# Performance work log

Measured on AMD Instinct MI355X. Metric: run time of the kernel, lower is better.

The kernel has to match this reference:

```python
import jax, jax.numpy as jnp
import numpy as np
from math import sqrt

N = 50000      # n_nodes
M = 800000     # n_edges (avg degree 16)
D = 256        # d_Embedding
H = 8          # heads
DK = 32        # per-head key/query dim
DV = 32        # per-head value dim


def setup_inputs() -> dict:
    key = jax.random.key(0)
    ks = jax.random.split(key, 10)
    s = 0.02
    x = jax.random.normal(ks[0], (N, D), dtype=jnp.float32)
    edge_index = jax.random.randint(ks[1], (2, M), 0, N, dtype=jnp.int32)
    # projection weights stored pre-reshaped to (D, H, dhead); equivalent to nn.Linear(D, H*dhead)
    Wk = jax.random.normal(ks[2], (D, H, DK), dtype=jnp.float32) * s
    bk = jax.random.normal(ks[3], (H, DK), dtype=jnp.float32) * s
    Wq = jax.random.normal(ks[4], (D, H, DK), dtype=jnp.float32) * s
    bq = jax.random.normal(ks[5], (H, DK), dtype=jnp.float32) * s
    Wv = jax.random.normal(ks[6], (D, H, DV), dtype=jnp.float32) * s
    bv = jax.random.normal(ks[7], (H, DV), dtype=jnp.float32) * s
    Wagg = jax.random.normal(ks[8], (H * DV, D), dtype=jnp.float32) * s
    bagg = jnp.zeros((D,), dtype=jnp.float32)
    Wff = jax.random.normal(ks[9], (D, D), dtype=jnp.float32) * s
    bff = jnp.zeros((D,), dtype=jnp.float32)
    return {"x": x, "edge_index": edge_index, "Wk": Wk, "bk": bk, "Wq": Wq,
            "bq": bq, "Wv": Wv, "bv": bv, "Wagg": Wagg, "bagg": bagg,
            "Wff": Wff, "bff": bff}


def reference(x, edge_index, Wk, bk, Wq, bq, Wv, bv, Wagg, bagg, Wff, bff):
    recv = edge_index[0]
    send = edge_index[1]
    # per-head projections: (N, H, d)
    K = jnp.einsum('nd,dhk->nhk', x, Wk) + bk
    Q = jnp.einsum('nd,dhk->nhk', x, Wq) + bq
    V = jnp.einsum('nd,dhv->nhv', x, Wv) + bv
    # edge-wise attention logits: (M, H)
    qk = jnp.sum(Q[recv] * K[send], axis=-1)
    # faithful to original: rescale by 3/global_max, then exp
    att = jnp.exp(qk * 3.0 / jnp.max(qk))
    # segment-softmax normalization over edges sharing a receiver
    sums = jax.ops.segment_sum(att, recv, num_segments=N)  # (N, H)
    att = att / sums[recv] / sqrt(DK)
    # weighted scatter-add of sender values: (N, H, DV)
    msg = att[..., None] * V[send]
    out = jax.ops.segment_sum(msg, recv, num_segments=N)
    out = jax.nn.relu(out).reshape(N, H * DV)
    out = jax.nn.relu(out @ Wagg + bagg)
    out = jax.nn.relu(out @ Wff + bff)
    return x + out
```

## Files before the change

kernel.cpp:

```cpp
#include <hip/hip_runtime.h>

#define N_NODES 50000
#define M_EDGES 800000
#define RP 50048

typedef __bf16 bf16x8 __attribute__((ext_vector_type(8)));
typedef __bf16 bf16x4 __attribute__((ext_vector_type(4)));
typedef float  f32x4  __attribute__((ext_vector_type(4)));

static __device__ __forceinline__ unsigned enc_ord(float f) {
    unsigned b = __float_as_uint(f);
    return (b & 0x80000000u) ? ~b : (b | 0x80000000u);
}
static __device__ __forceinline__ float dec_ord(unsigned u) {
    unsigned b = (u & 0x80000000u) ? (u ^ 0x80000000u) : ~u;
    return __uint_as_float(b);
}
static __device__ __forceinline__ float bflo(unsigned u) { return __uint_as_float(u << 16); }
static __device__ __forceinline__ float bfhi(unsigned u) { return __uint_as_float(u & 0xffff0000u); }

__global__ void init_kernel(int* counts, int* cursor, unsigned* gmax) {
    int t = blockIdx.x * blockDim.x + threadIdx.x;
    if (t < N_NODES) { counts[t] = 0; cursor[t] = 0; }
    if (t == 0) *gmax = 0u;
}

__global__ void wsplit_kernel(const float* __restrict__ W,
                              __bf16* __restrict__ th, __bf16* __restrict__ tl) {
    int t = blockIdx.x * 256 + threadIdx.x;
    int n = t >> 8, k = t & 255;
    float v = W[(size_t)k * 256 + n];
    __bf16 h = (__bf16)v;
    th[t] = h;
    tl[t] = (__bf16)(v - (float)h);
}

__global__ void xsplit_kernel(const float* __restrict__ X,
                              __bf16* __restrict__ xh, __bf16* __restrict__ xl) {
    size_t i = ((size_t)blockIdx.x * 256 + threadIdx.x) * 4;
    if (i >= (size_t)N_NODES * 256) return;
    float4 v = *(const float4*)(X + i);
    bf16x4 hh, ll;
    hh[0] = (__bf16)v.x; ll[0] = (__bf16)(v.x - (float)hh[0]);
    hh[1] = (__bf16)v.y; ll[1] = (__bf16)(v.y - (float)hh[1]);
    hh[2] = (__bf16)v.z; ll[2] = (__bf16)(v.z - (float)hh[2]);
    hh[3] = (__bf16)v.w; ll[3] = (__bf16)(v.w - (float)hh[3]);
    *(bf16x4*)(xh + i) = hh;
    *(bf16x4*)(xl + i) = ll;
}

__global__ __launch_bounds__(256) void gemm_mfma(
    const __bf16* __restrict__ Ah, const __bf16* __restrict__ Al,
    const __bf16* __restrict__ Bth, const __bf16* __restrict__ Btl,
    const float* __restrict__ bias, const float* __restrict__ residual,
    float* __restrict__ C, __bf16* __restrict__ CbH, __bf16* __restrict__ CbL,
    int nrows, int do_relu) {
    __shared__ __attribute__((aligned(16))) __bf16 sAh[128 * 40];
    __shared__ __attribute__((aligned(16))) __bf16 sAl[128 * 40];
    __shared__ __attribute__((aligned(16))) __bf16 sBh[128 * 40];
    __shared__ __attribute__((aligned(16))) __bf16 sBl[128 * 40];

    int row0 = blockIdx.x * 128;
    int n0   = blockIdx.y * 128;
    int tid  = threadIdx.x;
    int lane = tid & 63, wave = tid >> 6;
    int wm = (wave >> 1) * 64, wn = (wave & 1) * 64;

    f32x4 acc[4][4];
    #pragma unroll
    for (int i = 0; i < 4; i++)
        #pragma unroll
        for (int j = 0; j < 4; j++) acc[i][j] = (f32x4)(0.f);

    int r  = tid >> 1;
    int hf = tid & 1;
    bool valid = (row0 + r) < nrows;

    for (int kk = 0; kk < 256; kk += 32) {
        {
            size_t ga = (size_t)(row0 + r) * 256 + kk + hf * 16;
            uint4 z = make_uint4(0u, 0u, 0u, 0u);
            uint4 ah0 = valid ? *(const uint4*)(Ah + ga)     : z;
            uint4 ah1 = valid ? *(const uint4*)(Ah + ga + 8) : z;
            uint4 al0 = valid ? *(const uint4*)(Al + ga)     : z;
            uint4 al1 = valid ? *(const uint4*)(Al + ga + 8) : z;
            *(uint4*)&sAh[r * 40 + hf * 16]     = ah0;
            *(uint4*)&sAh[r * 40 + hf * 16 + 8] = ah1;
            *(uint4*)&sAl[r * 40 + hf * 16]     = al0;
            *(uint4*)&sAl[r * 40 + hf * 16 + 8] = al1;
        }
        {
            size_t gb = (size_t)(n0 + r) * 256 + kk + hf * 16;
            uint4 vh0 = *(const uint4*)(Bth + gb);
            uint4 vh1 = *(const uint4*)(Bth + gb + 8);
            uint4 vl0 = *(const uint4*)(Btl + gb);
            uint4 vl1 = *(const uint4*)(Btl + gb + 8);
            *(uint4*)&sBh[r * 40 + hf * 16]     = vh0;
            *(uint4*)&sBh[r * 40 + hf * 16 + 8] = vh1;
            *(uint4*)&sBl[r * 40 + hf * 16]     = vl0;
            *(uint4*)&sBl[r * 40 + hf * 16 + 8] = vl1;
        }
        __syncthreads();

        int m_base = wm + (lane & 15);
        int n_base = wn + (lane & 15);
        int koff = (lane >> 4) * 8;
        bf16x8 ah[4], al[4], bh[4], bl[4];
        #pragma unroll
        for (int mt = 0; mt < 4; mt++) {
            ah[mt] = *(const bf16x8*)&sAh[(m_base + mt * 16) * 40 + koff];
            al[mt] = *(const bf16x8*)&sAl[(m_base + mt * 16) * 40 + koff];
        }
        #pragma unroll
        for (int nt = 0; nt < 4; nt++) {
            bh[nt] = *(const bf16x8*)&sBh[(n_base + nt * 16) * 40 + koff];
            bl[nt] = *(const bf16x8*)&sBl[(n_base + nt * 16) * 40 + koff];
        }
        #pragma unroll
        for (int mt = 0; mt < 4; mt++)
            #pragma unroll
            for (int nt = 0; nt < 4; nt++) {
                acc[mt][nt] = __builtin_amdgcn_mfma_f32_16x16x32_bf16(ah[mt], bh[nt], acc[mt][nt], 0, 0, 0);
                acc[mt][nt] = __builtin_amdgcn_mfma_f32_16x16x32_bf16(al[mt], bh[nt], acc[mt][nt], 0, 0, 0);
                acc[mt][nt] = __builtin_amdgcn_mfma_f32_16x16x32_bf16(ah[mt], bl[nt], acc[mt][nt], 0, 0, 0);
            }
        __syncthreads();
    }

    #pragma unroll
    for (int mt = 0; mt < 4; mt++) {
        #pragma unroll
        for (int nt = 0; nt < 4; nt++) {
            int col = n0 + wn + nt * 16 + (lane & 15);
            #pragma unroll
            for (int rr = 0; rr < 4; rr++) {
                int row = row0 + wm + mt * 16 + (lane >> 4) * 4 + rr;
                if (row < nrows) {
                    float v = acc[mt][nt][rr] + bias[col];
                    if (do_relu) v = fmaxf(v, 0.f);
                    size_t idx = (size_t)row * 256 + col;
                    if (CbH) {
                        __bf16 hh = (__bf16)v;
                        CbH[idx] = hh;
                        if (CbL) CbL[idx] = (__bf16)(v - (float)hh);
                    } else {
                        if (residual) v += residual[idx];
                        C[idx] = v;
                    }
                }
            }
        }
    }
}

__global__ void hist_kernel(const int* __restrict__ recv, int* __restrict__ counts) {
    int t = blockIdx.x * 256 + threadIdx.x;
    if (t < M_EDGES) atomicAdd(&counts[recv[t]], 1);
}

__global__ void scan_kernel(const int* __restrict__ counts, int* __restrict__ offsets) {
    __shared__ int part[256];
    int t = threadIdx.x;
    const int per = (N_NODES + 255) / 256;
    int start = t * per;
    int end = min(start + per, N_NODES);
    int s = 0;
    for (int i = start; i < end; i++) s += counts[i];
    part[t] = s;
    __syncthreads();
    if (t == 0) {
        int acc = 0;
        for (int i = 0; i < 256; i++) { int v = part[i]; part[i] = acc; acc += v; }
    }
    __syncthreads();
    int acc = part[t];
    for (int i = start; i < end; i++) { offsets[i] = acc; acc += counts[i]; }
    if (end == N_NODES && start < N_NODES) offsets[N_NODES] = acc;
}

__global__ void fill_kernel(const int* __restrict__ recv, const int* __restrict__ send,
                            const int* __restrict__ offsets,
                            int* __restrict__ cursor, int* __restrict__ ssorted,
                            int* __restrict__ rsorted) {
    int t = blockIdx.x * 256 + threadIdx.x;
    if (t < M_EDGES) {
        int r = recv[t];
        int pos = offsets[r] + atomicAdd(&cursor[r], 1);
        ssorted[pos] = send[t];
        rsorted[pos] = r;
    }
}

__global__ __launch_bounds__(256) void qk_csr_kernel(
    const int* __restrict__ ssorted, const int* __restrict__ rsorted,
    const float* __restrict__ Q, const unsigned short* __restrict__ Kb,
    float* __restrict__ qks, unsigned* __restrict__ gmax) {
    int wave_id = (blockIdx.x * 256 + threadIdx.x) >> 6;
    int lane = threadIdx.x & 63;
    int e_slot = lane >> 5;
    int sl = lane & 31;
    const int nwaves = (gridDim.x * 256) >> 6;
    const int npairs = M_EDGES / 2;
    float wmax = -INFINITY;
    for (int pp = wave_id; pp < npairs; pp += 4 * nwaves) {
        int ep[4]; bool valid[4];
        #pragma unroll
        for (int u = 0; u < 4; u++) {
            int p = pp + u * nwaves;
            valid[u] = p < npairs;
            ep[u] = (valid[u] ? p : pp) * 2 + e_slot;
        }
        int si[4], ri[4];
        #pragma unroll
        for (int u = 0; u < 4; u++) { si[u] = ssorted[ep[u]]; ri[u] = rsorted[ep[u]]; }
        uint4 kv[4]; float4 qa[4], qb[4];
        #pragma unroll
        for (int u = 0; u < 4; u++) {
            kv[u] = *(const uint4*)(Kb + (size_t)si[u] * 256 + sl * 8);
            qa[u] = *(const float4*)(Q + (size_t)ri[u] * 256 + sl * 8);
            qb[u] = *(const float4*)(Q + (size_t)ri[u] * 256 + sl * 8 + 4);
        }
        #pragma unroll
        for (int u = 0; u < 4; u++) {
            float d = qa[u].x * bflo(kv[u].x) + qa[u].y * bfhi(kv[u].x)
                    + qa[u].z * bflo(kv[u].y) + qa[u].w * bfhi(kv[u].y)
                    + qb[u].x * bflo(kv[u].z) + qb[u].y * bfhi(kv[u].z)
                    + qb[u].z * bflo(kv[u].w) + qb[u].w * bfhi(kv[u].w);
            d += __shfl_xor(d, 1);
            d += __shfl_xor(d, 2);
            wmax = fmaxf(wmax, d);
            if ((sl & 3) == 0 && valid[u])
                qks[(size_t)ep[u] * 8 + (sl >> 2)] = d;
        }
    }
    wmax = fmaxf(wmax, __shfl_xor(wmax, 1));
    wmax = fmaxf(wmax, __shfl_xor(wmax, 2));
    wmax = fmaxf(wmax, __shfl_xor(wmax, 4));
    wmax = fmaxf(wmax, __shfl_xor(wmax, 8));
    wmax = fmaxf(wmax, __shfl_xor(wmax, 16));
    wmax = fmaxf(wmax, __shfl_xor(wmax, 32));
    if (lane == 0 && wmax > -INFINITY) atomicMax(gmax, enc_ord(wmax));
}

__global__ __launch_bounds__(256) void node_agg_kernel(
    const int* __restrict__ offsets, const int* __restrict__ ssorted,
    const float* __restrict__ qks, const unsigned short* __restrict__ Vb,
    const unsigned* __restrict__ gmax,
    __bf16* __restrict__ msgH, __bf16* __restrict__ msgL) {
    int wave_id = (blockIdx.x * 256 + threadIdx.x) >> 6;
    int lane = threadIdx.x & 63;
    int h = lane >> 3;
    const int nwaves = (gridDim.x * 256) >> 6;
    const int per = (N_NODES + nwaves - 1) / nwaves;
    int n0 = wave_id * per;
    int nend = min(n0 + per, N_NODES);
    float scale = 3.0f / dec_ord(*gmax);
    for (int n = n0; n < nend; n++) {
        int off = offsets[n];
        int deg = offsets[n + 1] - off;
        float sum = 0.f, a0 = 0.f, a1 = 0.f, a2 = 0.f, a3 = 0.f;
        for (int b = 0; b < deg; b += 64) {
            int bn = min(64, deg - b);
            int idxb = ssorted[off + b + min(lane, bn - 1)];
            #define VROW(i) (*(const uint2*)(Vb + \
                (size_t)__shfl(idxb, min((i), bn - 1)) * 256 + lane * 4))
            #define QKL(i) qks[(size_t)(off + b + min((i), bn - 1)) * 8 + h]
            uint2 v0 = VROW(0);
            uint2 v1 = VROW(1);
            float q0 = QKL(0);
            float q1 = QKL(1);
            for (int i = 0; i < bn; i++) {
                uint2 vc = v0; v0 = v1; v1 = VROW(i + 2);
                float qc = q0; q0 = q1; q1 = QKL(i + 2);
                float a = __expf(qc * scale);
                sum += a;
                a0 += a * bflo(vc.x); a1 += a * bfhi(vc.x);
                a2 += a * bflo(vc.y); a3 += a * bfhi(vc.y);
            }
            #undef VROW
            #undef QKL
        }
        float inv = (deg > 0) ? 1.0f / (sum * 5.65685424949238f) : 0.f;
        float r0 = fmaxf(a0 * inv, 0.f), r1 = fmaxf(a1 * inv, 0.f);
        float r2 = fmaxf(a2 * inv, 0.f), r3 = fmaxf(a3 * inv, 0.f);
        bf16x4 hv, lv;
        hv[0] = (__bf16)r0; lv[0] = (__bf16)(r0 - (float)hv[0]);
        hv[1] = (__bf16)r1; lv[1] = (__bf16)(r1 - (float)hv[1]);
        hv[2] = (__bf16)r2; lv[2] = (__bf16)(r2 - (float)hv[2]);
        hv[3] = (__bf16)r3; lv[3] = (__bf16)(r3 - (float)hv[3]);
        *(bf16x4*)(msgH + (size_t)n * 256 + lane * 4) = hv;
        *(bf16x4*)(msgL + (size_t)n * 256 + lane * 4) = lv;
    }
}

extern "C" void kernel_launch(void* const* d_in, const int* in_sizes, int n_in,
                              void* d_out, int out_size, void* d_ws, size_t ws_size,
                              hipStream_t stream) {
    const float* x    = (const float*)d_in[0];
    const int*   edge = (const int*)d_in[1];
    const int*   recv = edge;
    const int*   send = edge + M_EDGES;
    const float* Wk   = (const float*)d_in[2];
    const float* bk   = (const float*)d_in[3];
    const float* Wq   = (const float*)d_in[4];
    const float* bq   = (const float*)d_in[5];
    const float* Wv   = (const float*)d_in[6];
    const float* bv   = (const float*)d_in[7];
    const float* Wagg = (const float*)d_in[8];
    const float* bagg = (const float*)d_in[9];
    const float* Wff  = (const float*)d_in[10];
    const float* bff  = (const float*)d_in[11];
    float* out = (float*)d_out;

    float*  Qbuf  = (float*)d_ws;
    float*  reg2  = Qbuf + (size_t)RP * 256;
    float*  qks   = reg2 + (size_t)RP * 256;
    __bf16* Kbf   = (__bf16*)(qks + (size_t)M_EDGES * 8);
    __bf16* Vbf   = Kbf + (size_t)RP * 256;
    int* counts   = (int*)(Vbf + (size_t)RP * 256);
    int* cursor   = counts + N_NODES;
    int* offsets  = cursor + N_NODES;
    int* ssorted  = offsets + N_NODES + 1;
    unsigned* gmax = (unsigned*)(ssorted + M_EDGES);
    __bf16* wt    = (__bf16*)(gmax + 1);
    __bf16* WkH = wt;              __bf16* WkL = wt + 65536;
    __bf16* WqH = wt + 2 * 65536;  __bf16* WqL = wt + 3 * 65536;
    __bf16* WvH = wt + 4 * 65536;  __bf16* WvL = wt + 5 * 65536;
    __bf16* WaH = wt + 6 * 65536;  __bf16* WaL = wt + 7 * 65536;
    __bf16* WfH = wt + 8 * 65536;  __bf16* WfL = wt + 9 * 65536;
    __bf16* xh   = (__bf16*)reg2;
    __bf16* xl   = xh + (size_t)RP * 256;
    int*    rsorted = (int*)reg2;
    __bf16* msgH = (__bf16*)reg2;
    __bf16* msgL = msgH + (size_t)RP * 256;
    __bf16* hidH = (__bf16*)Qbuf;
    __bf16* hidL = hidH + (size_t)RP * 256;

    dim3 blk(256);
    dim3 gemm_grid((N_NODES + 127) / 128, 2);
    dim3 edge_grid((M_EDGES + 255) / 256);

    hipLaunchKernelGGL(init_kernel, dim3((N_NODES + 255) / 256), blk, 0, stream,
                       counts, cursor, gmax);
    hipLaunchKernelGGL(wsplit_kernel, dim3(256), blk, 0, stream, Wk,   WkH, WkL);
    hipLaunchKernelGGL(wsplit_kernel, dim3(256), blk, 0, stream, Wq,   WqH, WqL);
    hipLaunchKernelGGL(wsplit_kernel, dim3(256), blk, 0, stream, Wv,   WvH, WvL);
    hipLaunchKernelGGL(wsplit_kernel, dim3(256), blk, 0, stream, Wagg, WaH, WaL);
    hipLaunchKernelGGL(wsplit_kernel, dim3(256), blk, 0, stream, Wff,  WfH, WfL);
    hipLaunchKernelGGL(xsplit_kernel, dim3((N_NODES * 256 / 4 + 255) / 256), blk, 0,
                       stream, x, xh, xl);
    hipLaunchKernelGGL(gemm_mfma, gemm_grid, blk, 0, stream, xh, xl, WkH, WkL, bk,
                       nullptr, (float*)nullptr, Kbf, (__bf16*)nullptr, N_NODES, 0);
    hipLaunchKernelGGL(gemm_mfma, gemm_grid, blk, 0, stream, xh, xl, WqH, WqL, bq,
                       nullptr, Qbuf, (__bf16*)nullptr, (__bf16*)nullptr, N_NODES, 0);
    hipLaunchKernelGGL(gemm_mfma, gemm_grid, blk, 0, stream, xh, xl, WvH, WvL, bv,
                       nullptr, (float*)nullptr, Vbf, (__bf16*)nullptr, N_NODES, 0);
    hipLaunchKernelGGL(hist_kernel, edge_grid, blk, 0, stream, recv, counts);
    hipLaunchKernelGGL(scan_kernel, dim3(1), blk, 0, stream, counts, offsets);
    hipLaunchKernelGGL(fill_kernel, edge_grid, blk, 0, stream, recv, send, offsets,
                       cursor, ssorted, rsorted);
    hipLaunchKernelGGL(qk_csr_kernel, dim3(1024), blk, 0, stream,
                       ssorted, rsorted, Qbuf, (const unsigned short*)Kbf, qks, gmax);
    hipLaunchKernelGGL(node_agg_kernel, dim3(2048), blk, 0, stream,
                       offsets, ssorted, qks, (const unsigned short*)Vbf, gmax,
                       msgH, msgL);
    hipLaunchKernelGGL(gemm_mfma, gemm_grid, blk, 0, stream, msgH, msgL, WaH, WaL,
                       bagg, nullptr, (float*)nullptr, hidH, hidL, N_NODES, 1);
    hipLaunchKernelGGL(gemm_mfma, gemm_grid, blk, 0, stream, hidH, hidL, WfH, WfL,
                       bff, x, out, (__bf16*)nullptr, (__bf16*)nullptr, N_NODES, 1);
}
```

Before: 851.4 us.

## Double-buffer GEMM tiles with direct global-to-LDS async loads

The split-bf16 MFMA GEMM now stages A and B tiles through global_load_lds, which writes global memory straight into shared memory without passing through registers. It double-buffers these tiles so the loads for the next K step are issued while the current one is being multiplied. The shared-memory layout changes to a k-chunk-major arrangement that fits the 16-byte-per-lane direct loads. The row bounds check on A is gone, so the last block may read past nrows when nrows is not a multiple of 128. The shared-memory footprint also doubles.

```diff
diff --git a/kernel.cpp b/kernel.cpp
--- a/kernel.cpp
+++ b/kernel.cpp
@@ -18,6 +18,12 @@
 }
 static __device__ __forceinline__ float bflo(unsigned u) { return __uint_as_float(u << 16); }
 static __device__ __forceinline__ float bfhi(unsigned u) { return __uint_as_float(u & 0xffff0000u); }
+
+static __device__ __forceinline__ void gload16(const void* g, void* l) {
+    __builtin_amdgcn_global_load_lds(
+        (const __attribute__((address_space(1))) void*)g,
+        (__attribute__((address_space(3))) void*)l, 16, 0, 0);
+}
 
 __global__ void init_kernel(int* counts, int* cursor, unsigned* gmax) {
     int t = blockIdx.x * blockDim.x + threadIdx.x;
@@ -55,10 +61,7 @@
     const float* __restrict__ bias, const float* __restrict__ residual,
     float* __restrict__ C, __bf16* __restrict__ CbH, __bf16* __restrict__ CbL,
     int nrows, int do_relu) {
-    __shared__ __attribute__((aligned(16))) __bf16 sAh[128 * 40];
-    __shared__ __attribute__((aligned(16))) __bf16 sAl[128 * 40];
-    __shared__ __attribute__((aligned(16))) __bf16 sBh[128 * 40];
-    __shared__ __attribute__((aligned(16))) __bf16 sBl[128 * 40];
+    __shared__ __attribute__((aligned(16))) __bf16 sm[2][4][4][128][8];
 
     int row0 = blockIdx.x * 128;
     int n0   = blockIdx.y * 128;
@@ -72,60 +75,62 @@
         #pragma unroll
         for (int j = 0; j < 4; j++) acc[i][j] = (f32x4)(0.f);
 
-    int r  = tid >> 1;
-    int hf = tid & 1;
-    bool valid = (row0 + r) < nrows;
-
-    for (int kk = 0; kk < 256; kk += 32) {
-        {
-            size_t ga = (size_t)(row0 + r) * 256 + kk + hf * 16;
-            uint4 z = make_uint4(0u, 0u, 0u, 0u);
-            uint4 ah0 = valid ? *(const uint4*)(Ah + ga)     : z;
-            uint4 ah1 = valid ? *(const uint4*)(Ah + ga + 8) : z;
-            uint4 al0 = valid ? *(const uint4*)(Al + ga)     : z;
-            uint4 al1 = valid ? *(const uint4*)(Al + ga + 8) : z;
-            *(uint4*)&sAh[r * 40 + hf * 16]     = ah0;
-            *(uint4*)&sAh[r * 40 + hf * 16 + 8] = ah1;
-            *(uint4*)&sAl[r * 40 + hf * 16]     = al0;
-            *(uint4*)&sAl[r * 40 + hf * 16 + 8] = al1;
-        }
-        {
-            size_t gb = (size_t)(n0 + r) * 256 + kk + hf * 16;
-            uint4 vh0 = *(const uint4*)(Bth + gb);
-            uint4 vh1 = *(const uint4*)(Bth + gb + 8);
-            uint4 vl0 = *(const uint4*)(Btl + gb);
-            uint4 vl1 = *(const uint4*)(Btl + gb + 8);
-            *(uint4*)&sBh[r * 40 + hf * 16]     = vh0;
-            *(uint4*)&sBh[r * 40 + hf * 16 + 8] = vh1;
-            *(uint4*)&sBl[r * 40 + hf * 16]     = vl0;
-            *(uint4*)&sBl[r * 40 + hf * 16 + 8] = vl1;
-        }
-        __syncthreads();
-
-        int m_base = wm + (lane & 15);
-        int n_base = wn + (lane & 15);
-        int koff = (lane >> 4) * 8;
-        bf16x8 ah[4], al[4], bh[4], bl[4];
+    int srow = tid & 127;
+    int shi  = tid >> 7;
+    const __bf16* gA0 = Ah  + (size_t)(row0 + srow) * 256;
+    const __bf16* gA1 = Al  + (size_t)(row0 + srow) * 256;
+    const __bf16* gB0 = Bth + (size_t)(n0 + srow) * 256;
+    const __bf16* gB1 = Btl + (size_t)(n0 + srow) * 256;
+    char* lds0 = (char*)&sm[0][0][0][0][0];
+
+#define STAGE(buf, kk) do {                                                   \
+        int ke0 = (kk) + shi * 8;                                             \
+        int ke1 = (kk) + (2 + shi) * 8;                                       \
+        size_t lo0 = (size_t)(buf) * 32768 + (size_t)tid * 16;                \
+        size_t lo1 = lo0 + 4096;                                              \
+        gload16(gA0 + ke0, lds0 + lo0);                                       \
+        gload16(gA0 + ke1, lds0 + lo1);                                       \
+        gload16(gA1 + ke0, lds0 + 8192 + lo0);                                \
+        gload16(gA1 + ke1, lds0 + 8192 + lo1);                                \
+        gload16(gB0 + ke0, lds0 + 16384 + lo0);                               \
+        gload16(gB0 + ke1, lds0 + 16384 + lo1);                               \
+        gload16(gB1 + ke0, lds0 + 24576 + lo0);                               \
+        gload16(gB1 + ke1, lds0 + 24576 + lo1);                               \
+    } while (0)
+
+    STAGE(0, 0);
+    __syncthreads();
+
+    int h = lane >> 4;
+    int m_base = wm + (lane & 15);
+    int n_base = wn + (lane & 15);
+
+    for (int t = 0; t < 8; t++) {
+        int cur = t & 1;
+        if (t < 7) STAGE(cur ^ 1, (t + 1) * 32);
+
+        bf16x8 ahf[4], alf[4], bhf[4], blf[4];
         #pragma unroll
         for (int mt = 0; mt < 4; mt++) {
-            ah[mt] = *(const bf16x8*)&sAh[(m_base + mt * 16) * 40 + koff];
-            al[mt] = *(const bf16x8*)&sAl[(m_base + mt * 16) * 40 + koff];
+            ahf[mt] = *(const bf16x8*)&sm[cur][0][h][m_base + mt * 16][0];
+            alf[mt] = *(const bf16x8*)&sm[cur][1][h][m_base + mt * 16][0];
         }
         #pragma unroll
         for (int nt = 0; nt < 4; nt++) {
-            bh[nt] = *(const bf16x8*)&sBh[(n_base + nt * 16) * 40 + koff];
-            bl[nt] = *(const bf16x8*)&sBl[(n_base + nt * 16) * 40 + koff];
+            bhf[nt] = *(const bf16x8*)&sm[cur][2][h][n_base + nt * 16][0];
+            blf[nt] = *(const bf16x8*)&sm[cur][3][h][n_base + nt * 16][0];
         }
         #pragma unroll
         for (int mt = 0; mt < 4; mt++)
             #pragma unroll
             for (int nt = 0; nt < 4; nt++) {
-                acc[mt][nt] = __builtin_amdgcn_mfma_f32_16x16x32_bf16(ah[mt], bh[nt], acc[mt][nt], 0, 0, 0);
-                acc[mt][nt] = __builtin_amdgcn_mfma_f32_16x16x32_bf16(al[mt], bh[nt], acc[mt][nt], 0, 0, 0);
-                acc[mt][nt] = __builtin_amdgcn_mfma_f32_16x16x32_bf16(ah[mt], bl[nt], acc[mt][nt], 0, 0, 0);
+                acc[mt][nt] = __builtin_amdgcn_mfma_f32_16x16x32_bf16(ahf[mt], bhf[nt], acc[mt][nt], 0, 0, 0);
+                acc[mt][nt] = __builtin_amdgcn_mfma_f32_16x16x32_bf16(alf[mt], bhf[nt], acc[mt][nt], 0, 0, 0);
+                acc[mt][nt] = __builtin_amdgcn_mfma_f32_16x16x32_bf16(ahf[mt], blf[nt], acc[mt][nt], 0, 0, 0);
             }
         __syncthreads();
     }
+#undef STAGE
 
     #pragma unroll
     for (int mt = 0; mt < 4; mt++) {
```

Result: slower. 877.6 us (+3.1%).
